# Optimization experiments

Measured on AMD Instinct MI355X. Metric: run time of the kernel, lower is better.

Reference implementation:

```python
import jax, jax.numpy as jnp
import numpy as np

NUM_NODES = 2_000_000
NUM_DAGS = 20_000
F = 5    # num_node_features
E = 32   # embed_dim
H = 64   # mlp hidden dim


def setup_inputs() -> dict:
    key = jax.random.key(0)
    ks = jax.random.split(key, 9)
    x = jax.random.normal(ks[0], (NUM_NODES, F), dtype=jnp.float32)
    h_node = jax.random.normal(ks[1], (NUM_NODES, E), dtype=jnp.float32)
    # ptr: CSR-style segment boundaries, ptr[0]=0, ptr[-1]=NUM_NODES
    inner = jnp.sort(jax.random.randint(ks[2], (NUM_DAGS - 1,), 0, NUM_NODES))
    ptr = jnp.concatenate([jnp.zeros((1,), jnp.int64),
                           inner.astype(jnp.int64),
                           jnp.full((1,), NUM_NODES, jnp.int64)])
    d_in = F + E
    def lin(k, fan_in, fan_out):
        s = 1.0 / np.sqrt(fan_in)
        return jax.random.uniform(k, (fan_in, fan_out), jnp.float32, -s, s)
    W1 = lin(ks[3], d_in, H); b1 = jnp.zeros((H,), jnp.float32)
    W2 = lin(ks[4], H, H);    b2 = jnp.zeros((H,), jnp.float32)
    W3 = lin(ks[5], H, E);    b3 = jnp.zeros((E,), jnp.float32)
    return {"h_node": h_node, "x": x, "W1": W1, "b1": b1, "W2": W2,
            "b2": b2, "W3": W3, "b3": b3, "ptr": ptr}


def reference(h_node, x, W1, b1, W2, b2, W3, b3, ptr):
    # concat node features with node embeddings: [num_nodes, F+E]
    h = jnp.concatenate([x, h_node], axis=1)
    # MLP: Linear-ReLU-Linear-ReLU-Linear -> [num_nodes, E]
    h = jax.nn.relu(h @ W1 + b1)
    h = jax.nn.relu(h @ W2 + b2)
    h = h @ W3 + b3
    # segment_csr(reduce='sum') over ptr -> [num_dags, E]
    num_dags = ptr.shape[0] - 1
    lengths = jnp.diff(ptr)
    seg_ids = jnp.repeat(jnp.arange(num_dags), lengths,
                         total_repeat_length=h.shape[0])
    return jax.ops.segment_sum(h, seg_ids, num_segments=num_dags)
```

## Files before the change

### kernel.cpp

```cpp
#include <hip/hip_runtime.h>
#include <hip/hip_bf16.h>

typedef __bf16 bf16;
typedef __bf16 bf16x4 __attribute__((ext_vector_type(4)));
typedef __bf16 bf16x8 __attribute__((ext_vector_type(8)));
typedef float  floatx4 __attribute__((ext_vector_type(4)));

#define NUM_NODES 2000000
#define NUM_DAGS  20000
#define NE 32

#define MFMA(a, b, c) __builtin_amdgcn_mfma_f32_16x16x32_bf16((a), (b), (c), 0, 0, 0)

#define ROW_BYTES  144
#define TILE_BYTES (16 * ROW_BYTES)
#define WAVE_LDS   (4 * TILE_BYTES)
#define WCHUNK     512
#define NGROUPS    (WCHUNK / 64)
#define CHUNK      (4 * WCHUNK)

__device__ __forceinline__ int seg_of(const int* __restrict__ ptr, int n, int st) {
    int lo = 0, hi = NUM_DAGS;
    while (hi - lo > 1) {
        int mid = (lo + hi) >> 1;
        if (ptr[mid * st] <= n) lo = mid; else hi = mid;
    }
    return lo;
}

#define LOADG(gBase, A0, A1)                                                      \
    do {                                                                          \
        _Pragma("unroll")                                                         \
        for (int j_ = 0; j_ < 4; ++j_) {                                          \
            const int node_ = (gBase) + j_ * 16 + mr;                             \
            bf16x8 f_ = {};                                                       \
            bf16x8 g_ = {};                                                       \
            if (node_ < NUM_NODES) {                                              \
                const floatx4* hp_ =                                              \
                    (const floatx4*)(h_node + (size_t)node_ * 32 + q * 8);        \
                floatx4 v0_ = hp_[0], v1_ = hp_[1];                               \
                f_[0] = (bf16)v0_[0]; f_[1] = (bf16)v0_[1];                       \
                f_[2] = (bf16)v0_[2]; f_[3] = (bf16)v0_[3];                       \
                f_[4] = (bf16)v1_[0]; f_[5] = (bf16)v1_[1];                       \
                f_[6] = (bf16)v1_[2]; f_[7] = (bf16)v1_[3];                       \
                if (q == 0) {                                                     \
                    const float* xp_ = x + (size_t)node_ * 5;                     \
                    g_[0] = (bf16)xp_[0]; g_[1] = (bf16)xp_[1];                   \
                    g_[2] = (bf16)xp_[2]; g_[3] = (bf16)xp_[3];                   \
                    g_[4] = (bf16)xp_[4];                                         \
                    g_[5] = (bf16)1.0f;                   \
                }                                                                 \
            }                                                                     \
            A0[j_] = f_;                                                          \
            A1[j_] = g_;                                                          \
        }                                                                         \
    } while (0)

__global__ __launch_bounds__(256, 2)
void dag_mfma_kernel(const float* __restrict__ h_node,
                     const float* __restrict__ x,
                     const float* __restrict__ W1, const float* __restrict__ b1,
                     const float* __restrict__ W2, const float* __restrict__ b2,
                     const float* __restrict__ W3, const float* __restrict__ b3,
                     const int* __restrict__ ptr,
                     float* __restrict__ out) {
    __shared__ __align__(16) char sBuf[16 * TILE_BYTES];

    const int tid = threadIdx.x;
    const int w   = tid >> 6;
    const int l   = tid & 63;
    const int q   = l >> 4;
    const int mr  = l & 15;

    const int wStart = blockIdx.x * CHUNK + w * WCHUNK;
    if (wStart >= NUM_NODES) return;

    const int pstride = (ptr[NUM_DAGS] == NUM_NODES) ? 1 : 2;

    bf16x8 a0c[4], a1c[4];
    bf16x8 a0n[4] = {}, a1n[4] = {};
    LOADG(wStart, a0c, a1c);

    bf16x8 w1f[2][4], w2f[2][4], w3f[2][2];
    #pragma unroll
    for (int s = 0; s < 2; ++s) {
        #pragma unroll
        for (int mt = 0; mt < 4; ++mt) {
            #pragma unroll
            for (int j = 0; j < 8; ++j) {
                const int kk  = s * 32 + q * 8 + j;
                const int col = mt * 16 + mr;
                float v1;
                if      (kk < 32)  v1 = W1[(kk + 5) * 64 + col];
                else if (kk < 37)  v1 = W1[(kk - 32) * 64 + col];
                else if (kk == 37) v1 = b1[col];
                else               v1 = 0.0f;
                w1f[s][mt][j] = (bf16)v1;
                w2f[s][mt][j] = (bf16)W2[kk * 64 + col];
                if (mt < 2) w3f[s][mt][j] = (bf16)W3[kk * 32 + mt * 16 + mr];
            }
        }
    }
    floatx4 b2f[4], b3f[2];
    #pragma unroll
    for (int mt = 0; mt < 4; ++mt)
        b2f[mt] = *(const floatx4*)(b2 + mt * 16 + q * 4);
    b3f[0] = *(const floatx4*)(b3 + q * 4);
    b3f[1] = *(const floatx4*)(b3 + 16 + q * 4);

    int seg = seg_of(ptr, wStart, pstride);

    char* myBuf = sBuf + w * WAVE_LDS;

    for (int g = 0; g < NGROUPS; ++g) {
        const int gLo = wStart + g * 64;
        if (gLo >= NUM_NODES) break;

        if (g + 1 < NGROUPS) LOADG(gLo + 64, a0n, a1n);

        #pragma unroll
        for (int j = 0; j < 4; ++j) {
            floatx4 c[4] = {};
            #pragma unroll
            for (int mt = 0; mt < 4; ++mt) {
                c[mt] = MFMA(w1f[0][mt], a0c[j], c[mt]);
                c[mt] = MFMA(w1f[1][mt], a1c[j], c[mt]);
            }
            char* tb = myBuf + j * TILE_BYTES + mr * ROW_BYTES;
            #pragma unroll
            for (int mt = 0; mt < 4; ++mt) {
                bf16x4 v;
                v[0] = (bf16)fmaxf(c[mt][0], 0.0f);
                v[1] = (bf16)fmaxf(c[mt][1], 0.0f);
                v[2] = (bf16)fmaxf(c[mt][2], 0.0f);
                v[3] = (bf16)fmaxf(c[mt][3], 0.0f);
                *(bf16x4*)(tb + mt * 32 + q * 8) = v;
            }
        }

        #pragma unroll
        for (int j = 0; j < 4; ++j) {
            char* tb = myBuf + j * TILE_BYTES + mr * ROW_BYTES;
            bf16x8 h0 = *(const bf16x8*)(tb + q * 16);
            bf16x8 h1 = *(const bf16x8*)(tb + 64 + q * 16);
            floatx4 c[4];
            #pragma unroll
            for (int mt = 0; mt < 4; ++mt) {
                c[mt] = b2f[mt];
                c[mt] = MFMA(w2f[0][mt], h0, c[mt]);
                c[mt] = MFMA(w2f[1][mt], h1, c[mt]);
            }
            #pragma unroll
            for (int mt = 0; mt < 4; ++mt) {
                bf16x4 v;
                v[0] = (bf16)fmaxf(c[mt][0], 0.0f);
                v[1] = (bf16)fmaxf(c[mt][1], 0.0f);
                v[2] = (bf16)fmaxf(c[mt][2], 0.0f);
                v[3] = (bf16)fmaxf(c[mt][3], 0.0f);
                *(bf16x4*)(tb + mt * 32 + q * 8) = v;
            }
        }

        #pragma unroll
        for (int j = 0; j < 4; ++j) {
            char* tb = myBuf + j * TILE_BYTES + mr * ROW_BYTES;
            bf16x8 p0 = *(const bf16x8*)(tb + q * 16);
            bf16x8 p1 = *(const bf16x8*)(tb + 64 + q * 16);
            floatx4 d0 = b3f[0], d1 = b3f[1];
            d0 = MFMA(w3f[0][0], p0, d0);
            d0 = MFMA(w3f[1][0], p1, d0);
            d1 = MFMA(w3f[0][1], p0, d1);
            d1 = MFMA(w3f[1][1], p1, d1);
            *(floatx4*)(tb + q * 16)      = d0;
            *(floatx4*)(tb + 64 + q * 16) = d1;
        }

        {
            const int gEnd = (gLo + 64 < NUM_NODES) ? gLo + 64 : NUM_NODES;
            while (ptr[(seg + 1) * pstride] <= gLo) ++seg;
            int segLast = seg;
            while (ptr[(segLast + 1) * pstride] <= gEnd - 1) ++segLast;

            const int f  = l & 31;
            const int gg = l >> 5;
            const float* so = (const float*)myBuf;
            for (int s = seg + gg; s <= segLast; s += 2) {
                int lo = ptr[s * pstride];
                int hi = ptr[(s + 1) * pstride];
                if (lo < gLo) lo = gLo;
                if (hi > gEnd) hi = gEnd;
                float acc = 0.0f;
                for (int i = lo; i < hi; ++i) {
                    const int nl = i - gLo;
                    acc += so[(nl >> 4) * 576 + (nl & 15) * 36 + f];
                }
                if (hi > lo) atomicAdd(&out[s * NE + f], acc);
            }
            seg = segLast;
        }

        #pragma unroll
        for (int j = 0; j < 4; ++j) { a0c[j] = a0n[j]; a1c[j] = a1n[j]; }
    }
}

extern "C" void kernel_launch(void* const* d_in, const int* in_sizes, int n_in,
                              void* d_out, int out_size, void* d_ws, size_t ws_size,
                              hipStream_t stream) {
    const float* h_node = (const float*)d_in[0];
    const float* x      = (const float*)d_in[1];
    const float* W1     = (const float*)d_in[2];
    const float* b1     = (const float*)d_in[3];
    const float* W2     = (const float*)d_in[4];
    const float* b2     = (const float*)d_in[5];
    const float* W3     = (const float*)d_in[6];
    const float* b3     = (const float*)d_in[7];
    const int*   ptr    = (const int*)d_in[8];
    float* out          = (float*)d_out;

    hipMemsetAsync(out, 0, (size_t)out_size * sizeof(float), stream);

    const int grid = (NUM_NODES + CHUNK - 1) / CHUNK;
    dag_mfma_kernel<<<grid, 256, 0, stream>>>(h_node, x, W1, b1, W2, b2,
                                              W3, b3, ptr, out);
}
```

Before: 472.9 us.

## Reduce segment sums in registers and carry accumulators across node groups

Layer-3 MFMA outputs stay in registers and are no longer written to LDS. Per-segment partial sums are built by masking each node's contribution, then reduced with cross-lane shuffles. An accumulator is carried across 64-node groups, so one atomicAdd per segment per wave replaces atomics per group. This removes LDS stores and reloads plus many global atomics, at the cost of shuffle reductions at segment boundaries and a per-segment loop over all lanes.

```diff
diff --git a/kernel.cpp b/kernel.cpp
--- a/kernel.cpp
+++ b/kernel.cpp
@@ -110,6 +110,9 @@
 
     int seg = seg_of(ptr, wStart, pstride);
 
+    int accSeg = seg;
+    floatx4 accLo = {}, accHi = {};
+
     char* myBuf = sBuf + w * WAVE_LDS;
 
     for (int g = 0; g < NGROUPS; ++g) {
@@ -161,6 +164,7 @@
             }
         }
 
+        floatx4 dLo[4], dHi[4];
         #pragma unroll
         for (int j = 0; j < 4; ++j) {
             char* tb = myBuf + j * TILE_BYTES + mr * ROW_BYTES;
@@ -171,8 +175,7 @@
             d0 = MFMA(w3f[1][0], p1, d0);
             d1 = MFMA(w3f[0][1], p0, d1);
             d1 = MFMA(w3f[1][1], p1, d1);
-            *(floatx4*)(tb + q * 16)      = d0;
-            *(floatx4*)(tb + 64 + q * 16) = d1;
+            dLo[j] = d0; dHi[j] = d1;
         }
 
         {
@@ -181,26 +184,70 @@
             int segLast = seg;
             while (ptr[(segLast + 1) * pstride] <= gEnd - 1) ++segLast;
 
-            const int f  = l & 31;
-            const int gg = l >> 5;
-            const float* so = (const float*)myBuf;
-            for (int s = seg + gg; s <= segLast; s += 2) {
-                int lo = ptr[s * pstride];
-                int hi = ptr[(s + 1) * pstride];
-                if (lo < gLo) lo = gLo;
-                if (hi > gEnd) hi = gEnd;
-                float acc = 0.0f;
-                for (int i = lo; i < hi; ++i) {
-                    const int nl = i - gLo;
-                    acc += so[(nl >> 4) * 576 + (nl & 15) * 36 + f];
+            const bool fullOne = (seg == segLast) && (gEnd == gLo + 64);
+
+            for (int s = seg; s <= segLast; ++s) {
+                floatx4 pLo, pHi;
+                if (fullOne) {
+                    pLo = dLo[0] + dLo[1] + dLo[2] + dLo[3];
+                    pHi = dHi[0] + dHi[1] + dHi[2] + dHi[3];
+                } else {
+                    int lo = ptr[s * pstride];
+                    int hi = ptr[(s + 1) * pstride];
+                    if (hi > gEnd) hi = gEnd;
+                    if (hi <= lo) continue;
+                    pLo = (floatx4){0.f, 0.f, 0.f, 0.f};
+                    pHi = (floatx4){0.f, 0.f, 0.f, 0.f};
+                    #pragma unroll
+                    for (int j = 0; j < 4; ++j) {
+                        const int node = gLo + j * 16 + mr;
+                        if (node >= lo && node < hi) { pLo += dLo[j]; pHi += dHi[j]; }
+                    }
                 }
-                if (hi > lo) atomicAdd(&out[s * NE + f], acc);
+                if (s == accSeg) {
+                    accLo += pLo; accHi += pHi;
+                } else {
+                    #pragma unroll
+                    for (int m = 1; m <= 8; m <<= 1) {
+                        #pragma unroll
+                        for (int r = 0; r < 4; ++r) {
+                            accLo[r] += __shfl_xor(accLo[r], m, 64);
+                            accHi[r] += __shfl_xor(accHi[r], m, 64);
+                        }
+                    }
+                    if (mr == 0) {
+                        #pragma unroll
+                        for (int r = 0; r < 4; ++r) {
+                            atomicAdd(&out[accSeg * NE + q * 4 + r],      accLo[r]);
+                            atomicAdd(&out[accSeg * NE + 16 + q * 4 + r], accHi[r]);
+                        }
+                    }
+                    accLo = pLo; accHi = pHi; accSeg = s;
+                }
             }
             seg = segLast;
         }
 
         #pragma unroll
         for (int j = 0; j < 4; ++j) { a0c[j] = a0n[j]; a1c[j] = a1n[j]; }
+    }
+
+    {
+        #pragma unroll
+        for (int m = 1; m <= 8; m <<= 1) {
+            #pragma unroll
+            for (int r = 0; r < 4; ++r) {
+                accLo[r] += __shfl_xor(accLo[r], m, 64);
+                accHi[r] += __shfl_xor(accHi[r], m, 64);
+            }
+        }
+        if (mr == 0) {
+            #pragma unroll
+            for (int r = 0; r < 4; ++r) {
+                atomicAdd(&out[accSeg * NE + q * 4 + r],      accLo[r]);
+                atomicAdd(&out[accSeg * NE + 16 + q * 4 + r], accHi[r]);
+            }
+        }
     }
 }
 
```

Result: faster. 451.7 us (-4.5%).

## Accumulate segment sums in registers across tiles, fold b3 into init

Applied to the files above, without the earlier changes.

Replaces the LDS round trip and per-group scalar segment reduction with register accumulation of the layer-3 MFMA outputs per segment, flushed via cross-lane shuffles and atomics only when the segment changes. The b3 bias is moved into a new init kernel that writes length*b3 per segment instead of memset. It also raises the launch-bounds occupancy hint from 2 to 3 blocks per SM. This aims to cut LDS traffic and scalar loop work, but adds more frequent shuffle-reduction flushes at boundaries and may add register pressure under the tighter occupancy target.

```diff
diff --git a/kernel.cpp b/kernel.cpp
--- a/kernel.cpp
+++ b/kernel.cpp
@@ -56,7 +56,26 @@
         }                                                                         \
     } while (0)
 
-__global__ __launch_bounds__(256, 2)
+#define FLUSH()                                                            \
+    do {                                                                   \
+        _Pragma("unroll")                                                  \
+        for (int m_ = 1; m_ <= 8; m_ <<= 1) {                              \
+            _Pragma("unroll")                                              \
+            for (int r_ = 0; r_ < 4; ++r_) {                               \
+                accLo[r_] += __shfl_xor(accLo[r_], m_, 64);                \
+                accHi[r_] += __shfl_xor(accHi[r_], m_, 64);                \
+            }                                                              \
+        }                                                                  \
+        if (mr == 0) {                                                     \
+            _Pragma("unroll")                                              \
+            for (int r_ = 0; r_ < 4; ++r_) {                               \
+                atomicAdd(&out[accSeg * NE + q * 4 + r_],      accLo[r_]); \
+                atomicAdd(&out[accSeg * NE + 16 + q * 4 + r_], accHi[r_]); \
+            }                                                              \
+        }                                                                  \
+    } while (0)
+
+__global__ __launch_bounds__(256, 3)
 void dag_mfma_kernel(const float* __restrict__ h_node,
                      const float* __restrict__ x,
                      const float* __restrict__ W1, const float* __restrict__ b1,
@@ -101,14 +120,15 @@
             }
         }
     }
-    floatx4 b2f[4], b3f[2];
+    floatx4 b2f[4];
     #pragma unroll
     for (int mt = 0; mt < 4; ++mt)
         b2f[mt] = *(const floatx4*)(b2 + mt * 16 + q * 4);
-    b3f[0] = *(const floatx4*)(b3 + q * 4);
-    b3f[1] = *(const floatx4*)(b3 + 16 + q * 4);
 
     int seg = seg_of(ptr, wStart, pstride);
+
+    int accSeg = seg;
+    floatx4 accLo = {}, accHi = {};
 
     char* myBuf = sBuf + w * WAVE_LDS;
 
@@ -166,35 +186,39 @@
             char* tb = myBuf + j * TILE_BYTES + mr * ROW_BYTES;
             bf16x8 p0 = *(const bf16x8*)(tb + q * 16);
             bf16x8 p1 = *(const bf16x8*)(tb + 64 + q * 16);
-            floatx4 d0 = b3f[0], d1 = b3f[1];
+            floatx4 d0 = {}, d1 = {};
             d0 = MFMA(w3f[0][0], p0, d0);
             d0 = MFMA(w3f[1][0], p1, d0);
             d1 = MFMA(w3f[0][1], p0, d1);
             d1 = MFMA(w3f[1][1], p1, d1);
-            *(floatx4*)(tb + q * 16)      = d0;
-            *(floatx4*)(tb + 64 + q * 16) = d1;
-        }
-
-        {
-            const int gEnd = (gLo + 64 < NUM_NODES) ? gLo + 64 : NUM_NODES;
-            while (ptr[(seg + 1) * pstride] <= gLo) ++seg;
+
+            const int jLo = gLo + j * 16;
+            if (jLo >= NUM_NODES) break;
+            const int jEnd = (jLo + 16 < NUM_NODES) ? jLo + 16 : NUM_NODES;
+
+            while (ptr[(seg + 1) * pstride] <= jLo) ++seg;
             int segLast = seg;
-            while (ptr[(segLast + 1) * pstride] <= gEnd - 1) ++segLast;
-
-            const int f  = l & 31;
-            const int gg = l >> 5;
-            const float* so = (const float*)myBuf;
-            for (int s = seg + gg; s <= segLast; s += 2) {
-                int lo = ptr[s * pstride];
-                int hi = ptr[(s + 1) * pstride];
-                if (lo < gLo) lo = gLo;
-                if (hi > gEnd) hi = gEnd;
-                float acc = 0.0f;
-                for (int i = lo; i < hi; ++i) {
-                    const int nl = i - gLo;
-                    acc += so[(nl >> 4) * 576 + (nl & 15) * 36 + f];
+            while (ptr[(segLast + 1) * pstride] <= jEnd - 1) ++segLast;
+
+            if (seg == segLast && seg == accSeg) {
+                accLo += d0; accHi += d1;
+            } else {
+                const int node = jLo + mr;
+                for (int s = seg; s <= segLast; ++s) {
+                    int lo = ptr[s * pstride];
+                    int hi = ptr[(s + 1) * pstride];
+                    if (lo < jLo) lo = jLo;
+                    if (hi > jEnd) hi = jEnd;
+                    if (hi <= lo) continue;
+                    floatx4 pLo = {}, pHi = {};
+                    if (node >= lo && node < hi) { pLo = d0; pHi = d1; }
+                    if (s == accSeg) {
+                        accLo += pLo; accHi += pHi;
+                    } else {
+                        FLUSH();
+                        accLo = pLo; accHi = pHi; accSeg = s;
+                    }
                 }
-                if (hi > lo) atomicAdd(&out[s * NE + f], acc);
             }
             seg = segLast;
         }
@@ -202,6 +226,19 @@
         #pragma unroll
         for (int j = 0; j < 4; ++j) { a0c[j] = a0n[j]; a1c[j] = a1n[j]; }
     }
+
+    FLUSH();
+}
+
+__global__ __launch_bounds__(256)
+void init_out(const int* __restrict__ ptr, const float* __restrict__ b3,
+              float* __restrict__ out) {
+    const int i = blockIdx.x * 256 + threadIdx.x;
+    if (i >= NUM_DAGS * NE) return;
+    const int s = i >> 5, f = i & 31;
+    const int pst = (ptr[NUM_DAGS] == NUM_NODES) ? 1 : 2;
+    const int len = ptr[(s + 1) * pst] - ptr[s * pst];
+    out[i] = (float)len * b3[f];
 }
 
 extern "C" void kernel_launch(void* const* d_in, const int* in_sizes, int n_in,
@@ -218,7 +255,8 @@
     const int*   ptr    = (const int*)d_in[8];
     float* out          = (float*)d_out;
 
-    hipMemsetAsync(out, 0, (size_t)out_size * sizeof(float), stream);
+    const int initGrid = (NUM_DAGS * NE + 255) / 256;
+    init_out<<<initGrid, 256, 0, stream>>>(ptr, b3, out);
 
     const int grid = (NUM_NODES + CHUNK - 1) / CHUNK;
     dag_mfma_kernel<<<grid, 256, 0, stream>>>(h_node, x, W1, b1, W2, b2,
```

Result: slower. 590.0 us (+24.7%).
